# Performance work log

Measured on AMD Instinct MI355X. Metric: run time of the kernel, lower is better.

The kernel has to match this reference:

```python
import jax, jax.numpy as jnp
import numpy as np

B = 16384      # batch of states
N = 64         # neighbors per state -> x width = 5 + 2*N = 133
H = 128        # embed / hidden feature dim (num_inputs)
HID = 256      # actor/critic hidden size
OUT = 2        # action dim


def setup_inputs() -> dict:
    key = jax.random.key(0)
    ks = jax.random.split(key, 12)
    w = lambda k, shp: (jax.random.normal(k, shp, jnp.float32) * 0.1)
    b = lambda n: jnp.full((n,), 0.1, jnp.float32)
    return {
        "x": jax.random.normal(ks[0], (B, 5 + 2 * N), jnp.float32),
        # embbedLayer: Linear(2,128)
        "We": w(ks[1], (H, 2)), "be": b(H),
        # hlayer: Linear(128,128)
        "Wh": w(ks[2], (H, H)), "bh": b(H),
        # attentionLayer: Linear(256,1)
        "Wa": w(ks[3], (1, 2 * H)), "ba": b(1),
        # layer2: Linear(133,128)
        "W2": w(ks[4], (H, H + 5)), "b2": b(H),
        # critic: Linear(128,256) -> Linear(256,1)
        "Wc1": w(ks[5], (HID, H)), "bc1": b(HID),
        "Wc2": w(ks[6], (1, HID)), "bc2": b(1),
        # actor: Linear(128,256) -> Linear(256,2)
        "Wp1": w(ks[7], (HID, H)), "bp1": b(HID),
        "Wp2": w(ks[8], (OUT, HID)), "bp2": b(OUT),
        # log_std parameter (std=0.0 -> ones*0.0)
        "log_std": jnp.zeros((1, OUT), jnp.float32),
    }


def reference(x, We, be, Wh, bh, Wa, ba, W2, b2,
              Wc1, bc1, Wc2, bc2, Wp1, bp1, Wp2, bp2, log_std):
    Bn = x.shape[0]
    state_loc = x[:, :5]                       # [B,5]
    nb = x[:, 5:].reshape(Bn, -1, 2)           # [B,N,2] ragged loop flattened

    e = jax.nn.relu(jnp.einsum('bnd,hd->bnh', nb, We) + be)   # [B,N,H]
    em = jnp.mean(e, axis=1, keepdims=True)                    # [B,1,H]
    h = jax.nn.relu(jnp.einsum('bnh,oh->bno', e, Wh) + bh)     # [B,N,H]

    # attentionLayer(hstack(e, em)): split Wa into e-part and mean-part
    Wa_e, Wa_m = Wa[:, :H], Wa[:, H:]
    score = jax.nn.relu(
        jnp.einsum('bnh,oh->bno', e, Wa_e)
        + jnp.einsum('bkh,oh->bko', em, Wa_m)   # [B,1,1] broadcasts over N
        + ba
    )                                            # [B,N,1]
    attn = jax.nn.softmax(score, axis=1)         # softmax over neighbors
    mean_feature = jnp.mean(attn * h, axis=1)    # [B,H]

    t = jax.nn.relu(
        jnp.concatenate([state_loc, mean_feature], axis=1) @ W2.T + b2
    )                                            # [B,H]

    value = jax.nn.relu(t @ Wc1.T + bc1) @ Wc2.T + bc2   # [B,1]
    mu = jax.nn.relu(t @ Wp1.T + bp1) @ Wp2.T + bp2       # [B,2]
    std = jnp.broadcast_to(jnp.exp(log_std), mu.shape)    # [B,2]
    return mu, std, value
```

## Files before the change

kernel.cpp:

```cpp
#include <hip/hip_runtime.h>

#define BATCH 16384
#define XDIM  133
#define RPB   2
#define EROW  272
#define MB    64
#define CROW  336
#define TROW  272

#define WH_OFF   0
#define W2_OFF   16384
#define WC1_OFF  36864
#define WP1_OFF  69632
#define WA_OFF   102400
#define MFG_OFF  208896

typedef __attribute__((ext_vector_type(8))) _Float16 half8;
typedef __attribute__((ext_vector_type(2))) _Float16 half2v;
typedef __attribute__((ext_vector_type(4))) float    f32x4;
typedef __attribute__((ext_vector_type(4))) unsigned int uint4v;

__device__ __forceinline__ float relu(float v) { return fmaxf(v, 0.f); }
__device__ __forceinline__ unsigned short f2h(float f) {
    _Float16 h = (_Float16)f;
    return __builtin_bit_cast(unsigned short, h);
}
__device__ __forceinline__ half2v pk2h(float a, float b) {
    return __builtin_bit_cast(half2v, __builtin_amdgcn_cvt_pkrtz(a, b));
}

__global__ __launch_bounds__(256)
void ac_prep(const float* __restrict__ Wh, const float* __restrict__ W2,
             const float* __restrict__ Wc1, const float* __restrict__ Wp1,
             const float* __restrict__ Wa, unsigned short* __restrict__ wsH)
{
    const int idx = blockIdx.x * 256 + threadIdx.x;
    const int stride = gridDim.x * 256;
    for (int i = idx; i < 128*128; i += stride) wsH[WH_OFF + i] = f2h(Wh[i]);
    for (int i = idx; i < 128*160; i += stride) {
        int o = i / 160, ck = i - o*160;
        float w = (ck < 128) ? W2[o*XDIM + 5 + ck]
                             : ((ck < 133) ? W2[o*XDIM + (ck - 128)] : 0.f);
        wsH[W2_OFF + i] = f2h(w);
    }
    for (int i = idx; i < 256*128; i += stride) wsH[WC1_OFF + i] = f2h(Wc1[i]);
    for (int i = idx; i < 256*128; i += stride) wsH[WP1_OFF + i] = f2h(Wp1[i]);
    for (int i = idx; i < 128;     i += stride) wsH[WA_OFF  + i] = f2h(Wa[i]);
}

__global__ __launch_bounds__(256, 4)
void ac_attn(const float* __restrict__ x,
             const float* __restrict__ We,  const float* __restrict__ be,
             const float* __restrict__ bh,
             const float* __restrict__ Wa,  const float* __restrict__ ba,
             const unsigned short* __restrict__ wsH,
             char* __restrict__ mfG)
{
    __shared__ __align__(16) char  eH[RPB * 64 * EROW];
    __shared__ __align__(16) float xs[RPB][128];
    __shared__ __align__(16) float attnS[RPB][64];
    __shared__ __align__(16) float mfS[RPB][128];
    __shared__ __align__(16) float pS[4][64];
    __shared__            float cpart[4][RPB];

    const int tid  = threadIdx.x;
    const int lane = tid & 63;
    const int wave = tid >> 6;
    const int b0   = blockIdx.x * RPB;

    {
        int r = tid >> 7, c = tid & 127;
        xs[r][c] = x[(size_t)(b0 + r) * XDIM + 5 + c];
    }
    __syncthreads();

    {
        const int hp = lane;
        const int q  = wave;
        const float w00 = We[hp*4+0], w01 = We[hp*4+1];
        const float w10 = We[hp*4+2], w11 = We[hp*4+3];
        const float be0 = be[hp*2],   be1 = be[hp*2+1];
        const float wam0 = Wa[128 + hp*2], wam1 = Wa[128 + hp*2+1];
        #pragma unroll
        for (int r = 0; r < RPB; ++r) {
            float ca = 0.f;
            #pragma unroll
            for (int i = 0; i < 16; ++i) {
                int n = q*16 + i;
                float2 nb = *(const float2*)&xs[r][2*n];
                float e0 = relu(fmaf(nb.x, w00, fmaf(nb.y, w01, be0)));
                float e1 = relu(fmaf(nb.x, w10, fmaf(nb.y, w11, be1)));
                ca = fmaf(e0, wam0, fmaf(e1, wam1, ca));
                int row = r*64 + n;
                *(half2v*)(eH + row*EROW + (hp << 2)) = pk2h(e0, e1);
            }
            #pragma unroll
            for (int off = 1; off < 64; off <<= 1) ca += __shfl_xor(ca, off);
            if (lane == 0) cpart[wave][r] = ca;
        }
    }
    __syncthreads();

    {
        const int r  = wave & 1;
        const int kh = wave >> 1;
        const int n  = lane;
        const int row = r*64 + n;
        const half2v* wa = (const half2v*)(wsH + WA_OFF) + kh*32;
        float s = 0.f;
        #pragma unroll
        for (int k16 = 0; k16 < 8; ++k16) {
            half8 v = *(const half8*)(eH + row*EROW + kh*128 + k16*16);
            const half2v* v2 = (const half2v*)&v;
            #pragma unroll
            for (int j = 0; j < 4; ++j)
                s = __builtin_amdgcn_fdot2(v2[j], wa[k16*4 + j], s, false);
        }
        pS[wave][n] = s;
    }
    __syncthreads();

    if (wave < RPB) {
        const int r = wave;
        const int n = lane;
        float s = pS[r][n] + pS[2 + r][n];
        float c = (cpart[0][r] + cpart[1][r] + cpart[2][r] + cpart[3][r]) * (1.f/64.f) + ba[0];
        float sc = relu(s + c);
        float m = sc;
        #pragma unroll
        for (int off = 1; off < 64; off <<= 1) m = fmaxf(m, __shfl_xor(m, off));
        float p = __expf(sc - m);
        float sum = p;
        #pragma unroll
        for (int off = 1; off < 64; off <<= 1) sum += __shfl_xor(sum, off);
        attnS[r][n] = p / (sum * 64.f);
    }
    __syncthreads();

    {
        const int lo = lane & 15;
        const int g  = lane >> 4;
        const int c0 = wave*32 + lo;
        const int c1 = c0 + 16;
        const unsigned short* WhH = wsH + WH_OFF;
        half8 bfr[2][4];
        #pragma unroll
        for (int kk = 0; kk < 4; ++kk) {
            int kb = kk*32 + g*8;
            bfr[0][kk] = *(const half8*)(WhH + c0*128 + kb);
            bfr[1][kk] = *(const half8*)(WhH + c1*128 + kb);
        }
        const float bh0 = bh[c0], bh1 = bh[c1];

        #pragma unroll
        for (int r = 0; r < RPB; ++r) {
            float mf0 = 0.f, mf1 = 0.f;
            #pragma unroll
            for (int nt = 0; nt < 4; ++nt) {
                const int arow = r*64 + nt*16 + lo;
                half8 af[4];
                #pragma unroll
                for (int kk = 0; kk < 4; ++kk)
                    af[kk] = *(const half8*)(eH + arow*EROW + kk*64 + g*16);
                f32x4 acc0 = {0.f, 0.f, 0.f, 0.f};
                f32x4 acc1 = {0.f, 0.f, 0.f, 0.f};
                #pragma unroll
                for (int kk = 0; kk < 4; ++kk) {
                    acc0 = __builtin_amdgcn_mfma_f32_16x16x32_f16(af[kk], bfr[0][kk], acc0, 0, 0, 0);
                    acc1 = __builtin_amdgcn_mfma_f32_16x16x32_f16(af[kk], bfr[1][kk], acc1, 0, 0, 0);
                }
                f32x4 at4 = *(const f32x4*)&attnS[r][nt*16 + g*4];
                #pragma unroll
                for (int j = 0; j < 4; ++j) {
                    mf0 = fmaf(at4[j], relu(acc0[j] + bh0), mf0);
                    mf1 = fmaf(at4[j], relu(acc1[j] + bh1), mf1);
                }
            }
            mf0 += __shfl_xor(mf0, 16);  mf0 += __shfl_xor(mf0, 32);
            mf1 += __shfl_xor(mf1, 16);  mf1 += __shfl_xor(mf1, 32);
            if (lane < 16) {
                mfS[r][wave*32 + lane]      = mf0;
                mfS[r][wave*32 + 16 + lane] = mf1;
            }
        }
    }
    __syncthreads();

    if (tid < RPB * 64) {
        int r = tid >> 6, c = tid & 63;
        *(half2v*)(mfG + ((size_t)(b0 + r) * 128 + 2*c) * 2) = pk2h(mfS[r][2*c], mfS[r][2*c+1]);
    }
}

__global__ __launch_bounds__(256, 1)
void ac_heads(const float* __restrict__ x, const char* __restrict__ mfG,
              const unsigned short* __restrict__ wsH,
              const float* __restrict__ b2,
              const float* __restrict__ bc1, const float* __restrict__ Wc2,
              const float* __restrict__ bc2,
              const float* __restrict__ bp1, const float* __restrict__ Wp2,
              const float* __restrict__ bp2,
              const float* __restrict__ log_std,
              float* __restrict__ out)
{
    __shared__ __align__(16) char catS[MB * CROW];
    __shared__ __align__(16) char tS[MB * TROW];
    __shared__ float redV [2][MB];
    __shared__ float redM0[2][MB];
    __shared__ float redM1[2][MB];

    const int tid  = threadIdx.x;
    const int lane = tid & 63;
    const int wave = tid >> 6;
    const int lo   = lane & 15;
    const int g    = lane >> 4;
    const int b0   = blockIdx.x * MB;

    for (int i = tid * 16; i < MB * CROW; i += 256 * 16)
        *(uint4v*)(catS + i) = (uint4v){0, 0, 0, 0};
    __syncthreads();
    for (int c = tid; c < MB * 16; c += 256) {
        int row = c >> 4, sl = c & 15;
        uint4v v = *(const uint4v*)(mfG + (size_t)(b0 + row) * 256 + sl * 16);
        *(uint4v*)(catS + row * CROW + sl * 16) = v;
    }
    for (int m = tid; m < MB; m += 256) {
        const float* xr = x + (size_t)(b0 + m) * XDIM;
        #pragma unroll
        for (int k = 0; k < 5; ++k)
            *(unsigned short*)(catS + m * CROW + 256 + 2*k) = f2h(xr[k]);
    }
    __syncthreads();

    {
        const int o = wave * 32 + lo;
        const unsigned short* W2H = wsH + W2_OFF;
        half8 bw[2][5];
        #pragma unroll
        for (int nt2 = 0; nt2 < 2; ++nt2)
            #pragma unroll
            for (int kk = 0; kk < 5; ++kk)
                bw[nt2][kk] = *(const half8*)(W2H + (size_t)(o + nt2*16)*160 + kk*32 + g*8);
        const float bb0 = b2[o], bb1 = b2[o + 16];
        #pragma unroll
        for (int mt = 0; mt < 4; ++mt) {
            const int arow = mt*16 + lo;
            half8 af[5];
            #pragma unroll
            for (int kk = 0; kk < 5; ++kk)
                af[kk] = *(const half8*)(catS + arow*CROW + kk*64 + g*16);
            f32x4 a0 = {0.f,0.f,0.f,0.f}, a1 = {0.f,0.f,0.f,0.f};
            #pragma unroll
            for (int kk = 0; kk < 5; ++kk) {
                a0 = __builtin_amdgcn_mfma_f32_16x16x32_f16(af[kk], bw[0][kk], a0, 0, 0, 0);
                a1 = __builtin_amdgcn_mfma_f32_16x16x32_f16(af[kk], bw[1][kk], a1, 0, 0, 0);
            }
            #pragma unroll
            for (int j = 0; j < 4; ++j) {
                int m = mt*16 + g*4 + j;
                *(unsigned short*)(tS + m*TROW + o*2)      = f2h(relu(a0[j] + bb0));
                *(unsigned short*)(tS + m*TROW + (o+16)*2) = f2h(relu(a1[j] + bb1));
            }
        }
    }
    __syncthreads();

    {
        const bool isval = (wave < 2);
        const unsigned short* W1H = wsH + (isval ? WC1_OFF : WP1_OFF);
        const float* bb = isval ? bc1 : bp1;
        const int obase = (wave & 1) * 128;
        float sA[4][4], sB[4][4];
        #pragma unroll
        for (int mt = 0; mt < 4; ++mt)
            #pragma unroll
            for (int j = 0; j < 4; ++j) { sA[mt][j] = 0.f; sB[mt][j] = 0.f; }

        #pragma unroll
        for (int np = 0; np < 4; ++np) {
            const int oA = obase + np*32 + lo;
            const int oB = oA + 16;
            half8 bf0[4], bf1[4];
            #pragma unroll
            for (int kk = 0; kk < 4; ++kk) {
                bf0[kk] = *(const half8*)(W1H + (size_t)oA*128 + kk*32 + g*8);
                bf1[kk] = *(const half8*)(W1H + (size_t)oB*128 + kk*32 + g*8);
            }
            const float biasA = bb[oA], biasB = bb[oB];
            float wA0, wB0, wA1 = 0.f, wB1 = 0.f;
            if (isval) { wA0 = Wc2[oA]; wB0 = Wc2[oB]; }
            else       { wA0 = Wp2[oA]; wB0 = Wp2[oB]; wA1 = Wp2[256+oA]; wB1 = Wp2[256+oB]; }

            #pragma unroll
            for (int mt = 0; mt < 4; ++mt) {
                const int arow = mt*16 + lo;
                half8 af[4];
                #pragma unroll
                for (int kk = 0; kk < 4; ++kk)
                    af[kk] = *(const half8*)(tS + arow*TROW + kk*64 + g*16);
                f32x4 a0 = {0.f,0.f,0.f,0.f}, a1 = {0.f,0.f,0.f,0.f};
                #pragma unroll
                for (int kk = 0; kk < 4; ++kk) {
                    a0 = __builtin_amdgcn_mfma_f32_16x16x32_f16(af[kk], bf0[kk], a0, 0, 0, 0);
                    a1 = __builtin_amdgcn_mfma_f32_16x16x32_f16(af[kk], bf1[kk], a1, 0, 0, 0);
                }
                #pragma unroll
                for (int j = 0; j < 4; ++j) {
                    float uA = relu(a0[j] + biasA);
                    float uB = relu(a1[j] + biasB);
                    sA[mt][j] += wA0*uA + wB0*uB;
                    sB[mt][j] += wA1*uA + wB1*uB;
                }
            }
        }
        #pragma unroll
        for (int mt = 0; mt < 4; ++mt)
            #pragma unroll
            for (int j = 0; j < 4; ++j) {
                #pragma unroll
                for (int off = 1; off < 16; off <<= 1) {
                    sA[mt][j] += __shfl_xor(sA[mt][j], off);
                    sB[mt][j] += __shfl_xor(sB[mt][j], off);
                }
            }
        if (lo == 0) {
            #pragma unroll
            for (int mt = 0; mt < 4; ++mt)
                #pragma unroll
                for (int j = 0; j < 4; ++j) {
                    int m = mt*16 + g*4 + j;
                    if (isval) redV[wave][m] = sA[mt][j];
                    else { redM0[wave-2][m] = sA[mt][j]; redM1[wave-2][m] = sB[mt][j]; }
                }
        }
    }
    __syncthreads();

    if (tid < MB) {
        const int m = tid;
        const int b = b0 + m;
        out[b*2 + 0]           = redM0[0][m] + redM0[1][m] + bp2[0];
        out[b*2 + 1]           = redM1[0][m] + redM1[1][m] + bp2[1];
        out[2*BATCH + b*2 + 0] = expf(log_std[0]);
        out[2*BATCH + b*2 + 1] = expf(log_std[1]);
        out[4*BATCH + b]       = redV[0][m] + redV[1][m] + bc2[0];
    }
}

extern "C" void kernel_launch(void* const* d_in, const int* in_sizes, int n_in,
                              void* d_out, int out_size, void* d_ws, size_t ws_size,
                              hipStream_t stream) {
    (void)in_sizes; (void)n_in; (void)ws_size; (void)out_size;
    const float* x       = (const float*)d_in[0];
    const float* We      = (const float*)d_in[1];
    const float* be      = (const float*)d_in[2];
    const float* Wh      = (const float*)d_in[3];
    const float* bh      = (const float*)d_in[4];
    const float* Wa      = (const float*)d_in[5];
    const float* ba      = (const float*)d_in[6];
    const float* W2      = (const float*)d_in[7];
    const float* b2      = (const float*)d_in[8];
    const float* Wc1     = (const float*)d_in[9];
    const float* bc1     = (const float*)d_in[10];
    const float* Wc2     = (const float*)d_in[11];
    const float* bc2     = (const float*)d_in[12];
    const float* Wp1     = (const float*)d_in[13];
    const float* bp1     = (const float*)d_in[14];
    const float* Wp2     = (const float*)d_in[15];
    const float* bp2     = (const float*)d_in[16];
    const float* log_std = (const float*)d_in[17];

    unsigned short* wsH = (unsigned short*)d_ws;
    char* mfG = (char*)d_ws + MFG_OFF;

    hipLaunchKernelGGL(ac_prep, dim3(64), dim3(256), 0, stream,
                       Wh, W2, Wc1, Wp1, Wa, wsH);
    hipLaunchKernelGGL(ac_attn, dim3(BATCH / RPB), dim3(256), 0, stream,
                       x, We, be, bh, Wa, ba, wsH, mfG);
    hipLaunchKernelGGL(ac_heads, dim3(BATCH / MB), dim3(256), 0, stream,
                       x, mfG, wsH, b2, bc1, Wc2, bc2, bp1, Wp2, bp2,
                       log_std, (float*)d_out);
}
```

Before: 81.16 us.

## Double attn block to 512 threads, packed fp16 embedding math, direct mf stores

The attention kernel now runs 512 threads (8 waves) per block, so each wave handles a single row or quarter-row instead of looping over both rows. The embedding layer is computed with packed half2 FMA and fdot2 using pre-packed We/be/Wa weights prepared in ac_prep. The mean-feature shared buffer and its extra barrier are dropped in favour of storing fp16 results straight to global memory. The aim is more parallelism and fewer instructions per thread, at the cost of fp16 precision in the embedding and narrower, uncoalesced 2-byte global stores.

```diff
diff --git a/kernel.cpp b/kernel.cpp
--- a/kernel.cpp
+++ b/kernel.cpp
@@ -13,9 +13,11 @@
 #define WC1_OFF  36864
 #define WP1_OFF  69632
 #define WA_OFF   102400
+#define WE2_OFF  102528
 #define MFG_OFF  208896
 
 typedef __attribute__((ext_vector_type(8))) _Float16 half8;
+typedef __attribute__((ext_vector_type(4))) _Float16 half4v;
 typedef __attribute__((ext_vector_type(2))) _Float16 half2v;
 typedef __attribute__((ext_vector_type(4))) float    f32x4;
 typedef __attribute__((ext_vector_type(4))) unsigned int uint4v;
@@ -32,7 +34,8 @@
 __global__ __launch_bounds__(256)
 void ac_prep(const float* __restrict__ Wh, const float* __restrict__ W2,
              const float* __restrict__ Wc1, const float* __restrict__ Wp1,
-             const float* __restrict__ Wa, unsigned short* __restrict__ wsH)
+             const float* __restrict__ Wa, const float* __restrict__ We,
+             const float* __restrict__ be, unsigned short* __restrict__ wsH)
 {
     const int idx = blockIdx.x * 256 + threadIdx.x;
     const int stride = gridDim.x * 256;
@@ -46,58 +49,71 @@
     for (int i = idx; i < 256*128; i += stride) wsH[WC1_OFF + i] = f2h(Wc1[i]);
     for (int i = idx; i < 256*128; i += stride) wsH[WP1_OFF + i] = f2h(Wp1[i]);
     for (int i = idx; i < 128;     i += stride) wsH[WA_OFF  + i] = f2h(Wa[i]);
-}
-
-__global__ __launch_bounds__(256, 4)
+    for (int hp = idx; hp < 128;   hp += stride) {
+        wsH[WE2_OFF + hp*8 + 0] = f2h(We[4*hp+0]);
+        wsH[WE2_OFF + hp*8 + 1] = f2h(We[4*hp+2]);
+        wsH[WE2_OFF + hp*8 + 2] = f2h(We[4*hp+1]);
+        wsH[WE2_OFF + hp*8 + 3] = f2h(We[4*hp+3]);
+        wsH[WE2_OFF + hp*8 + 4] = f2h(be[2*hp+0]);
+        wsH[WE2_OFF + hp*8 + 5] = f2h(be[2*hp+1]);
+        wsH[WE2_OFF + hp*8 + 6] = f2h(Wa[128+2*hp+0]);
+        wsH[WE2_OFF + hp*8 + 7] = f2h(Wa[128+2*hp+1]);
+    }
+}
+
+__global__ __launch_bounds__(512, 6)
 void ac_attn(const float* __restrict__ x,
-             const float* __restrict__ We,  const float* __restrict__ be,
-             const float* __restrict__ bh,
-             const float* __restrict__ Wa,  const float* __restrict__ ba,
+             const float* __restrict__ bh,  const float* __restrict__ ba,
              const unsigned short* __restrict__ wsH,
              char* __restrict__ mfG)
 {
     __shared__ __align__(16) char  eH[RPB * 64 * EROW];
-    __shared__ __align__(16) float xs[RPB][128];
+    __shared__ __align__(16) char  xsH[RPB * 64 * 8];
     __shared__ __align__(16) float attnS[RPB][64];
-    __shared__ __align__(16) float mfS[RPB][128];
-    __shared__ __align__(16) float pS[4][64];
-    __shared__            float cpart[4][RPB];
+    __shared__ __align__(16) float pS[8][64];
+    __shared__            float cpart[8];
 
     const int tid  = threadIdx.x;
     const int lane = tid & 63;
     const int wave = tid >> 6;
     const int b0   = blockIdx.x * RPB;
 
-    {
-        int r = tid >> 7, c = tid & 127;
-        xs[r][c] = x[(size_t)(b0 + r) * XDIM + 5 + c];
+    if (tid < 128) {
+        int r = tid >> 6, n = tid & 63;
+        float2 nb = *(const float2*)(x + (size_t)(b0 + r) * XDIM + 5 + 2*n);
+        half2v s0 = pk2h(nb.x, nb.x);
+        half2v s1 = pk2h(nb.y, nb.y);
+        half4v s; s[0] = s0[0]; s[1] = s0[1]; s[2] = s1[0]; s[3] = s1[1];
+        *(half4v*)(xsH + (r*64 + n)*8) = s;
     }
     __syncthreads();
 
     {
         const int hp = lane;
-        const int q  = wave;
-        const float w00 = We[hp*4+0], w01 = We[hp*4+1];
-        const float w10 = We[hp*4+2], w11 = We[hp*4+3];
-        const float be0 = be[hp*2],   be1 = be[hp*2+1];
-        const float wam0 = Wa[128 + hp*2], wam1 = Wa[128 + hp*2+1];
-        #pragma unroll
-        for (int r = 0; r < RPB; ++r) {
-            float ca = 0.f;
-            #pragma unroll
-            for (int i = 0; i < 16; ++i) {
-                int n = q*16 + i;
-                float2 nb = *(const float2*)&xs[r][2*n];
-                float e0 = relu(fmaf(nb.x, w00, fmaf(nb.y, w01, be0)));
-                float e1 = relu(fmaf(nb.x, w10, fmaf(nb.y, w11, be1)));
-                ca = fmaf(e0, wam0, fmaf(e1, wam1, ca));
-                int row = r*64 + n;
-                *(half2v*)(eH + row*EROW + (hp << 2)) = pk2h(e0, e1);
-            }
-            #pragma unroll
-            for (int off = 1; off < 64; off <<= 1) ca += __shfl_xor(ca, off);
-            if (lane == 0) cpart[wave][r] = ca;
-        }
+        const int r  = wave >> 2;
+        const int nq = wave & 3;
+        half8 wp = *(const half8*)(wsH + WE2_OFF + hp*8);
+        half2v W0 = {wp[0], wp[1]};
+        half2v W1 = {wp[2], wp[3]};
+        half2v BE = {wp[4], wp[5]};
+        half2v WAM = {wp[6], wp[7]};
+        const half2v Z = {(_Float16)0.0f, (_Float16)0.0f};
+        float ca = 0.f;
+        #pragma unroll
+        for (int i = 0; i < 16; ++i) {
+            int n = nq*16 + i;
+            half4v s = *(const half4v*)(xsH + (r*64 + n)*8);
+            half2v s0 = {s[0], s[1]};
+            half2v s1 = {s[2], s[3]};
+            half2v X = s0*W0 + BE;
+            X = s1*W1 + X;
+            X = __builtin_elementwise_max(X, Z);
+            ca = __builtin_amdgcn_fdot2(X, WAM, ca, false);
+            *(half2v*)(eH + (r*64 + n)*EROW + (hp << 2)) = X;
+        }
+        #pragma unroll
+        for (int off = 1; off < 64; off <<= 1) ca += __shfl_xor(ca, off);
+        if (lane == 0) cpart[wave] = ca;
     }
     __syncthreads();
 
@@ -106,11 +122,11 @@
         const int kh = wave >> 1;
         const int n  = lane;
         const int row = r*64 + n;
-        const half2v* wa = (const half2v*)(wsH + WA_OFF) + kh*32;
+        const half2v* wa = (const half2v*)(wsH + WA_OFF) + kh*16;
         float s = 0.f;
         #pragma unroll
-        for (int k16 = 0; k16 < 8; ++k16) {
-            half8 v = *(const half8*)(eH + row*EROW + kh*128 + k16*16);
+        for (int k16 = 0; k16 < 4; ++k16) {
+            half8 v = *(const half8*)(eH + row*EROW + kh*64 + k16*16);
             const half2v* v2 = (const half2v*)&v;
             #pragma unroll
             for (int j = 0; j < 4; ++j)
@@ -120,11 +136,11 @@
     }
     __syncthreads();
 
-    if (wave < RPB) {
+    if (wave < 2) {
         const int r = wave;
         const int n = lane;
-        float s = pS[r][n] + pS[2 + r][n];
-        float c = (cpart[0][r] + cpart[1][r] + cpart[2][r] + cpart[3][r]) * (1.f/64.f) + ba[0];
+        float s = pS[r][n] + pS[2 + r][n] + pS[4 + r][n] + pS[6 + r][n];
+        float c = (cpart[r*4+0] + cpart[r*4+1] + cpart[r*4+2] + cpart[r*4+3]) * (1.f/64.f) + ba[0];
         float sc = relu(s + c);
         float m = sc;
         #pragma unroll
@@ -140,7 +156,9 @@
     {
         const int lo = lane & 15;
         const int g  = lane >> 4;
-        const int c0 = wave*32 + lo;
+        const int r  = wave >> 2;
+        const int cs = wave & 3;
+        const int c0 = cs*32 + lo;
         const int c1 = c0 + 16;
         const unsigned short* WhH = wsH + WH_OFF;
         half8 bfr[2][4];
@@ -152,43 +170,35 @@
         }
         const float bh0 = bh[c0], bh1 = bh[c1];
 
-        #pragma unroll
-        for (int r = 0; r < RPB; ++r) {
-            float mf0 = 0.f, mf1 = 0.f;
-            #pragma unroll
-            for (int nt = 0; nt < 4; ++nt) {
-                const int arow = r*64 + nt*16 + lo;
-                half8 af[4];
-                #pragma unroll
-                for (int kk = 0; kk < 4; ++kk)
-                    af[kk] = *(const half8*)(eH + arow*EROW + kk*64 + g*16);
-                f32x4 acc0 = {0.f, 0.f, 0.f, 0.f};
-                f32x4 acc1 = {0.f, 0.f, 0.f, 0.f};
-                #pragma unroll
-                for (int kk = 0; kk < 4; ++kk) {
-                    acc0 = __builtin_amdgcn_mfma_f32_16x16x32_f16(af[kk], bfr[0][kk], acc0, 0, 0, 0);
-                    acc1 = __builtin_amdgcn_mfma_f32_16x16x32_f16(af[kk], bfr[1][kk], acc1, 0, 0, 0);
-                }
-                f32x4 at4 = *(const f32x4*)&attnS[r][nt*16 + g*4];
-                #pragma unroll
-                for (int j = 0; j < 4; ++j) {
-                    mf0 = fmaf(at4[j], relu(acc0[j] + bh0), mf0);
-                    mf1 = fmaf(at4[j], relu(acc1[j] + bh1), mf1);
-                }
-            }
-            mf0 += __shfl_xor(mf0, 16);  mf0 += __shfl_xor(mf0, 32);
-            mf1 += __shfl_xor(mf1, 16);  mf1 += __shfl_xor(mf1, 32);
-            if (lane < 16) {
-                mfS[r][wave*32 + lane]      = mf0;
-                mfS[r][wave*32 + 16 + lane] = mf1;
-            }
-        }
-    }
-    __syncthreads();
-
-    if (tid < RPB * 64) {
-        int r = tid >> 6, c = tid & 63;
-        *(half2v*)(mfG + ((size_t)(b0 + r) * 128 + 2*c) * 2) = pk2h(mfS[r][2*c], mfS[r][2*c+1]);
+        float mf0 = 0.f, mf1 = 0.f;
+        #pragma unroll
+        for (int nt = 0; nt < 4; ++nt) {
+            const int arow = r*64 + nt*16 + lo;
+            half8 af[4];
+            #pragma unroll
+            for (int kk = 0; kk < 4; ++kk)
+                af[kk] = *(const half8*)(eH + arow*EROW + kk*64 + g*16);
+            f32x4 acc0 = {0.f, 0.f, 0.f, 0.f};
+            f32x4 acc1 = {0.f, 0.f, 0.f, 0.f};
+            #pragma unroll
+            for (int kk = 0; kk < 4; ++kk) {
+                acc0 = __builtin_amdgcn_mfma_f32_16x16x32_f16(af[kk], bfr[0][kk], acc0, 0, 0, 0);
+                acc1 = __builtin_amdgcn_mfma_f32_16x16x32_f16(af[kk], bfr[1][kk], acc1, 0, 0, 0);
+            }
+            f32x4 at4 = *(const f32x4*)&attnS[r][nt*16 + g*4];
+            #pragma unroll
+            for (int j = 0; j < 4; ++j) {
+                mf0 = fmaf(at4[j], relu(acc0[j] + bh0), mf0);
+                mf1 = fmaf(at4[j], relu(acc1[j] + bh1), mf1);
+            }
+        }
+        mf0 += __shfl_xor(mf0, 16);  mf0 += __shfl_xor(mf0, 32);
+        mf1 += __shfl_xor(mf1, 16);  mf1 += __shfl_xor(mf1, 32);
+        if (lane < 16) {
+            size_t base = (size_t)(b0 + r) * 128 + cs*32 + lane;
+            *(unsigned short*)(mfG + base*2)        = f2h(mf0);
+            *(unsigned short*)(mfG + (base + 16)*2) = f2h(mf1);
+        }
     }
 }
 
@@ -374,9 +384,9 @@
     char* mfG = (char*)d_ws + MFG_OFF;
 
     hipLaunchKernelGGL(ac_prep, dim3(64), dim3(256), 0, stream,
-                       Wh, W2, Wc1, Wp1, Wa, wsH);
-    hipLaunchKernelGGL(ac_attn, dim3(BATCH / RPB), dim3(256), 0, stream,
-                       x, We, be, bh, Wa, ba, wsH, mfG);
+                       Wh, W2, Wc1, Wp1, Wa, We, be, wsH);
+    hipLaunchKernelGGL(ac_attn, dim3(BATCH / RPB), dim3(512), 0, stream,
+                       x, bh, ba, wsH, mfG);
     hipLaunchKernelGGL(ac_heads, dim3(BATCH / MB), dim3(256), 0, stream,
                        x, mfG, wsH, b2, bc1, Wc2, bc2, bp1, Wp2, bp2,
                        log_std, (float*)d_out);
```

After: 112.8 us. +39.0%, slower.
